# Performance work log

Hardware: AMD Instinct MI355X
Metric: run time of the kernel (lower is better)

## Reference

```python
import jax, jax.numpy as jnp
import numpy as np

STATE_DIM = 16
MEAS_DIM = 8
T = 500_000


def setup_inputs() -> dict:
    key = jax.random.key(0)
    k1, k2 = jax.random.split(key)
    measurements = jax.random.normal(k1, (T, MEAS_DIM, 1), dtype=jnp.float32)
    # F contracted slightly below identity so the 500k-step recursion stays stable
    F = 0.95 * jnp.eye(STATE_DIM, dtype=jnp.float32) \
        + 0.01 * jax.random.normal(k2, (STATE_DIM, STATE_DIM), dtype=jnp.float32)
    H = jnp.eye(MEAS_DIM, STATE_DIM, dtype=jnp.float32)  # matches nn.Parameter(torch.eye(m, n))
    Q = jnp.eye(STATE_DIM, dtype=jnp.float32)
    R = jnp.eye(MEAS_DIM, dtype=jnp.float32)
    return {"measurements": measurements, "F": F, "H": H, "Q": Q, "R": R}


def reference(measurements, F, H, Q, R):
    n = F.shape[0]
    I = jnp.eye(n, dtype=F.dtype)
    x0 = jnp.zeros((n, 1), dtype=F.dtype)   # self.x init
    P0 = jnp.eye(n, dtype=F.dtype)          # self.P init

    def step(carry, z):
        x, P = carry
        # predict
        x = F @ x
        P = F @ P @ F.T + Q
        # update
        y = z - H @ x                         # (m,1) innovation
        S = H @ P @ H.T + R                   # (m,m) innovation covariance
        K = P @ H.T @ jnp.linalg.inv(S)       # (n,m) Kalman gain (faithful to torch.linalg.inv)
        x = x + K @ y
        P = (I - K @ H) @ P
        return (x, P), x

    _, states = jax.lax.scan(step, (x0, P0), measurements)
    return states  # (T, n, 1)
```

## Files before the change

### kernel.cpp

```cpp
#include <hip/hip_runtime.h>


#define TT 500000
#define T0 40
#define L1 32
#define NCHUNK 15624
#define GH 8
#define OWN 64
#define NBLK2 245
#define NTHR (16 * (GH + OWN/2))

#define OFF_A    0
#define OFF_KR   256
#define OFF_AL   512
#define OFF_KH   784

#define FENCE_LDS() do { \
  asm volatile("s_waitcnt lgkmcnt(0)" ::: "memory"); \
  __builtin_amdgcn_sched_barrier(0); \
} while (0)

#define FMACDPP(d, x, a, S) \
  asm("v_fmac_f32_dpp %0, %1, %2 row_ror:" #S " row_mask:0xf bank_mask:0xf" \
      : "+v"(d) : "v"(x), "v"(a))
#define MULDPPD(d, x, a, dep, S) \
  asm("v_mul_f32_dpp %0, %1, %2 row_ror:" #S " row_mask:0xf bank_mask:0xf" \
      : "=v"(d) : "v"(x), "v"(a), "v"(dep))

__device__ __forceinline__ float rlf(float v, int lane) {
  return __int_as_float(__builtin_amdgcn_readlane(__float_as_int(v), lane));
}
__device__ __forceinline__ float bpermf(int byteaddr, float v) {
  return __int_as_float(__builtin_amdgcn_ds_bpermute(byteaddr, __float_as_int(v)));
}
template<int CTL> __device__ __forceinline__ float dppf(float x) {
  return __int_as_float(__builtin_amdgcn_update_dpp(
      0, __float_as_int(x), CTL, 0xF, 0xF, false));
}
#define QP1 0x39
#define QP2 0x4E
#define QP3 0x93

__device__ __forceinline__ unsigned long long rtclock() {
  unsigned long long t;
  asm volatile("s_memrealtime %0\n\ts_waitcnt lgkmcnt(0)" : "=s"(t));
  return t;
}

__device__ __forceinline__ int rot_dir() {
  int r = threadIdx.x & 15;
  int m = __builtin_amdgcn_update_dpp(0, r, 0x121, 0xF, 0xF, false);
  return (m - r) & 15;
}
__device__ __forceinline__ float mv16(const float a[16], float x) {
  float s0 = a[0] * x;
  float s1, s2, s3;
  MULDPPD(s1, x, a[1], s0, 1);
  MULDPPD(s2, x, a[2], s0, 2);
  MULDPPD(s3, x, a[3], s0, 3);
  FMACDPP(s0, x, a[4], 4);   FMACDPP(s1, x, a[5], 5);
  FMACDPP(s2, x, a[6], 6);   FMACDPP(s3, x, a[7], 7);
  FMACDPP(s0, x, a[8], 8);   FMACDPP(s1, x, a[9], 9);
  FMACDPP(s2, x, a[10], 10); FMACDPP(s3, x, a[11], 11);
  FMACDPP(s0, x, a[12], 12); FMACDPP(s1, x, a[13], 13);
  FMACDPP(s2, x, a[14], 14); FMACDPP(s3, x, a[15], 15);
  return (s0 + s1) + (s2 + s3);
}
__device__ __forceinline__ float stepAK(const float a[16], const float k8[8],
                                        float u, float zv) {
  float s0 = __builtin_fmaf(k8[0], zv, a[0] * u);
  float s1, s2, s3;
  MULDPPD(s1, u, a[1], s0, 1);
  MULDPPD(s2, u, a[2], s0, 2);
  MULDPPD(s3, u, a[3], s0, 3);
  FMACDPP(s0, u, a[4], 4);   FMACDPP(s1, u, a[5], 5);
  FMACDPP(s2, u, a[6], 6);   FMACDPP(s3, u, a[7], 7);
  FMACDPP(s0, u, a[8], 8);   FMACDPP(s1, u, a[9], 9);
  FMACDPP(s2, u, a[10], 10); FMACDPP(s3, u, a[11], 11);
  FMACDPP(s0, u, a[12], 12); FMACDPP(s1, u, a[13], 13);
  FMACDPP(s2, u, a[14], 14); FMACDPP(s3, u, a[15], 15);
  FMACDPP(s1, zv, k8[1], 1); FMACDPP(s2, zv, k8[2], 2);
  FMACDPP(s3, zv, k8[3], 3); FMACDPP(s0, zv, k8[4], 4);
  FMACDPP(s1, zv, k8[5], 5); FMACDPP(s2, zv, k8[6], 6);
  FMACDPP(s3, zv, k8[7], 7);
  return (s0 + s1) + (s2 + s3);
}
__device__ __forceinline__ void load16(const float* p, int r, float d[16]) {
  #pragma unroll
  for (int j = 0; j < 4; ++j) {
    float4 t = ((const float4*)p)[r*4 + j];
    d[4*j] = t.x; d[4*j+1] = t.y; d[4*j+2] = t.z; d[4*j+3] = t.w;
  }
}
__device__ __forceinline__ void loadkrf(const float* p, int r, float k8[8]) {
  float kr[16];
  load16(p, r, kr);
  #pragma unroll
  for (int i = 0; i < 8; ++i) k8[i] = kr[i] + kr[i + 8];
}
__device__ __forceinline__ void loadz(const float* __restrict__ z, int s0_,
                                      int rr, float zr[L1]) {
  const float* zp = z + (size_t)s0_ * 8 + (rr & 7);
  if (s0_ + L1 <= TT) {
    #pragma unroll
    for (int t = 0; t < L1; ++t) zr[t] = zp[t * 8];
  } else {
    #pragma unroll
    for (int t = 0; t < L1; ++t) {
      const float* q = (s0_ + t < TT) ? (zp + t * 8) : z;
      zr[t] = *q;
    }
  }
}

__global__ __launch_bounds__(64) void kf_ricc(
    const float* __restrict__ Fg, const float* __restrict__ Qg,
    const float* __restrict__ Rg, float* __restrict__ ws)
{
  const int bid = blockIdx.x;
  if (bid != 0) {
    unsigned long long t0c = rtclock();
    float x = 1.0f + (float)threadIdx.x * 1e-7f;
    #pragma unroll 1
    for (int it = 0; it < 250; ++it) {
      #pragma unroll
      for (int j = 0; j < 48; ++j)
        x = __builtin_fmaf(x, 1.0000001f, 1e-30f);
      if (rtclock() - t0c > 4000ull) break;
    }
    asm volatile("" :: "v"(x));
    return;
  }

  const int l  = threadIdx.x;
  const int r4 = l >> 2;
  const int q  = l & 3;
  const int c4 = q * 4;
  const int dir = rot_dir();

  __shared__ float Ps[16][20], Pbs[16][20], Ms[16][20];
  __shared__ float KsL[16][8];

  float frow[16];
  #pragma unroll
  for (int k = 0; k < 16; ++k) frow[k] = Fg[r4*16 + k];
  float4 ftr[16];
  #pragma unroll
  for (int d = 0; d < 4; ++d) {
    #pragma unroll
    for (int jp = 0; jp < 4; ++jp) {
      int col = 4*((q + d) & 3) + jp;
      ftr[d*4+jp] = make_float4(Fg[(c4+0)*16 + col], Fg[(c4+1)*16 + col],
                                Fg[(c4+2)*16 + col], Fg[(c4+3)*16 + col]);
    }
  }
  float4 qreg = *(const float4*)&Qg[r4*16 + c4];
  float rcol[8];
  {
    int cc = l & 7;
    #pragma unroll
    for (int i = 0; i < 8; ++i) rcol[i] = Rg[i*8 + cc];
  }
  *(float4*)&Ps[r4][c4] = make_float4(r4==c4 ?1.f:0.f, r4==c4+1?1.f:0.f,
                                      r4==c4+2?1.f:0.f, r4==c4+3?1.f:0.f);
  const int  cidx = (l < 8) ? l : ((l < 24) ? (l - 8) : (l & 7));
  const bool isS  = (l < 8);
  const bool isB  = (l >= 8 && l < 24);
  const int  bj   = l - 8;
  const int  ba   = (8 + r4) << 2;
  float v[8];
  FENCE_LDS();

  for (int t = 0; t < T0; ++t) {
    float m0=0.f,m1=0.f,m2=0.f,m3=0.f;
    #pragma unroll
    for (int k = 0; k < 16; ++k) {
      float4 pk = *(const float4*)&Ps[k][c4];
      float f = frow[k];
      m0 += f*pk.x; m1 += f*pk.y; m2 += f*pk.z; m3 += f*pk.w;
    }
    float g1x=dppf<QP1>(m0), g1y=dppf<QP1>(m1), g1z=dppf<QP1>(m2), g1w=dppf<QP1>(m3);
    float g2x=dppf<QP2>(m0), g2y=dppf<QP2>(m1), g2z=dppf<QP2>(m2), g2w=dppf<QP2>(m3);
    float g3x=dppf<QP3>(m0), g3y=dppf<QP3>(m1), g3z=dppf<QP3>(m2), g3w=dppf<QP3>(m3);
    const float mq[4][4] = {{m0,m1,m2,m3},{g1x,g1y,g1z,g1w},
                            {g2x,g2y,g2z,g2w},{g3x,g3y,g3z,g3w}};
    float b0=qreg.x, b1=qreg.y, b2=qreg.z, b3=qreg.w;
    #pragma unroll
    for (int d = 0; d < 4; ++d) {
      #pragma unroll
      for (int jp = 0; jp < 4; ++jp) {
        float mm = mq[d][jp];
        float4 ft = ftr[d*4+jp];
        b0 += mm*ft.x; b1 += mm*ft.y; b2 += mm*ft.z; b3 += mm*ft.w;
      }
    }
    float4 pb = make_float4(b0,b1,b2,b3);
    *(float4*)&Pbs[r4][c4] = pb;
    FENCE_LDS();
    #pragma unroll
    for (int i = 0; i < 8; ++i)
      v[i] = Pbs[i][cidx] + (isS ? rcol[i] : 0.f);
    #pragma unroll
    for (int p = 0; p < 8; ++p) {
      float piv = rlf(v[p], p);
      float rc  = __builtin_amdgcn_rcpf(piv);
      float fi[8];
      #pragma unroll
      for (int i = 0; i < 8; ++i) fi[i] = rlf(v[i], p) * rc;
      #pragma unroll
      for (int i = 0; i < 8; ++i) if (i != p) v[i] -= fi[i] * v[p];
    }
    {
      float dv[8];
      #pragma unroll
      for (int i = 0; i < 8; ++i) dv[i] = __builtin_amdgcn_rcpf(rlf(v[i], i));
      #pragma unroll
      for (int i = 0; i < 8; ++i) v[i] *= dv[i];
    }
    if (isB) {
      #pragma unroll
      for (int i = 0; i < 8; ++i) ws[OFF_KH + t*128 + bj*8 + i] = v[i];
    }
    float kk[8];
    #pragma unroll
    for (int i = 0; i < 8; ++i) kk[i] = bpermf(ba, v[i]);
    float4 pn = pb;
    #pragma unroll
    for (int k = 0; k < 8; ++k) {
      float4 pr = *(const float4*)&Pbs[k][c4];
      float kv = kk[k];
      pn.x -= kv*pr.x; pn.y -= kv*pr.y; pn.z -= kv*pr.z; pn.w -= kv*pr.w;
    }
    *(float4*)&Ps[r4][c4] = pn;
    FENCE_LDS();
  }

  if (isB) {
    #pragma unroll
    for (int i = 0; i < 8; ++i) KsL[bj][i] = v[i];
  }
  float kk[8];
  #pragma unroll
  for (int i = 0; i < 8; ++i) kk[i] = bpermf(ba, v[i]);
  float a[4];
  #pragma unroll
  for (int j = 0; j < 4; ++j) {
    float s = Fg[r4*16 + c4 + j];
    #pragma unroll
    for (int k = 0; k < 8; ++k) s -= kk[k] * Fg[k*16 + c4 + j];
    a[j] = s;
  }
  *(float4*)&Ms[r4][c4] = make_float4(a[0],a[1],a[2],a[3]);
  #pragma unroll
  for (int j = 0; j < 4; ++j) {
    int c = c4 + j;
    int s = ((c - r4) * dir) & 15;
    ws[OFF_A + r4*16 + s] = a[j];
  }
  FENCE_LDS();
  if (l < 16) {
    #pragma unroll
    for (int s = 0; s < 16; ++s) {
      int c = (l + s*dir) & 15;
      ws[OFF_KR + l*16 + s] = (c < 8) ? KsL[l][c] : 0.f;
    }
  }
  FENCE_LDS();
  for (int n = 0; n < 5; ++n) {
    float (*src)[20] = (n & 1) ? Pbs : Ms;
    float (*dst)[20] = (n & 1) ? Ms : Pbs;
    float b[4] = {0.f, 0.f, 0.f, 0.f};
    #pragma unroll
    for (int k = 0; k < 16; ++k) {
      float m = src[r4][k];
      const float* p = &src[k][c4];
      b[0] += m*p[0]; b[1] += m*p[1]; b[2] += m*p[2]; b[3] += m*p[3];
    }
    FENCE_LDS();
    dst[r4][c4]=b[0]; dst[r4][c4+1]=b[1]; dst[r4][c4+2]=b[2]; dst[r4][c4+3]=b[3];
    FENCE_LDS();
    if (n == 4) {
      #pragma unroll
      for (int j = 0; j < 4; ++j) {
        int c = c4 + j;
        int s = ((c - r4) * dir) & 15;
        ws[OFF_AL + r4*16 + s] = b[j];
      }
    }
  }
}

__global__ __launch_bounds__(NTHR) void kf_scan(
    const float* __restrict__ z, const float* __restrict__ Fg,
    float* __restrict__ ws, float* __restrict__ out)
{
  const int tid = threadIdx.x;
  const int bid = blockIdx.x;
  const int r = tid & 15;
  const int g = tid >> 4;

  __shared__ float ueL[(GH + OWN) * 16];
  __shared__ float X0s[16];

  float a[16], krf[8];
  load16(&ws[OFF_A], r, a);
  loadkrf(&ws[OFF_KR], r, krf);

  float zrA[L1], zrB[L1];
  int cA = -1, cB = -1, lenB = 0, s0A = 0, s0B = 0;

  if (g < GH) {
    if (bid == 0) {
      if (g == 0) {
        float f[16];
        #pragma unroll
        for (int i = 0; i < 16; ++i) f[i] = Fg[r*16 + i];
        const float4* zb = (const float4*)z + r;
        const float4* kh = (const float4*)&ws[OFF_KH] + r*2;
        float x = 0.f;
        float4 d0 = zb[0], d1 = zb[16];
        float4 ka0 = kh[0],  kb0 = kh[1];
        float4 ka1 = kh[32], kb1 = kh[33];
        for (int b = 0; b < T0/8; ++b) {
          float4 nx = (b + 2 < T0/8) ? zb[(b+2)*16] : make_float4(0.f,0.f,0.f,0.f);
          #pragma unroll
          for (int j = 0; j < 8; ++j) {
            const int t = b*8 + j;
            float p0=0.f,p1=0.f,p2=0.f,p3=0.f;
            #pragma unroll
            for (int k = 0; k < 16; k += 4) {
              p0 += f[k]   * __shfl(x, k, 16);
              p1 += f[k+1] * __shfl(x, k+1, 16);
              p2 += f[k+2] * __shfl(x, k+2, 16);
              p3 += f[k+3] * __shfl(x, k+3, 16);
            }
            float xp = (p0+p1)+(p2+p3);
            float z0=__shfl(d0.x,2*j,16),   z1=__shfl(d0.y,2*j,16);
            float z2=__shfl(d0.z,2*j,16),   z3=__shfl(d0.w,2*j,16);
            float z4=__shfl(d0.x,2*j+1,16), z5=__shfl(d0.y,2*j+1,16);
            float z6=__shfl(d0.z,2*j+1,16), z7=__shfl(d0.w,2*j+1,16);
            float acc = xp;
            acc += ka0.x * (z0 - __shfl(xp,0,16));
            acc += ka0.y * (z1 - __shfl(xp,1,16));
            acc += ka0.z * (z2 - __shfl(xp,2,16));
            acc += ka0.w * (z3 - __shfl(xp,3,16));
            acc += kb0.x * (z4 - __shfl(xp,4,16));
            acc += kb0.y * (z5 - __shfl(xp,5,16));
            acc += kb0.z * (z6 - __shfl(xp,6,16));
            acc += kb0.w * (z7 - __shfl(xp,7,16));
            x = acc;
            out[t*16 + r] = x;
            ka0 = ka1; kb0 = kb1;
            if (t + 2 < T0) { ka1 = kh[(t+2)*32]; kb1 = kh[(t+2)*32 + 1]; }
          }
          d0 = d1; d1 = nx;
        }
        X0s[r] = x;
      }
    } else {
      int cg = bid*OWN - GH + g;
      int s0_ = T0 + cg*L1;
      loadz(z, s0_, r, zrA);
      float u = 0.f;
      #pragma unroll
      for (int t = 0; t < L1; ++t) u = stepAK(a, krf, u, zrA[t]);
      ueL[g*16 + r] = u;
    }
  } else {
    int k = g - GH;
    cA = bid*OWN + 2*k;
    if (cA < NCHUNK) {
      s0A = T0 + cA*L1;
      loadz(z, s0A, r, zrA);
      float u = 0.f;
      #pragma unroll
      for (int t = 0; t < L1; ++t) {
        u = stepAK(a, krf, u, zrA[t]);
        zrA[t] = u;
      }
      ueL[(GH + 2*k)*16 + r] = u;
      cB = cA + 1;
      if (cB < NCHUNK) {
        s0B = s0A + L1;
        lenB = min(s0B + L1, TT) - s0B;
        loadz(z, s0B, r, zrB);
        u = 0.f;
        #pragma unroll
        for (int t = 0; t < L1; ++t) {
          if (t >= lenB) break;
          u = stepAK(a, krf, u, zrB[t]);
          zrB[t] = u;
        }
        ueL[(GH + 2*k + 1)*16 + r] = u;
      }
    } else {
      cA = -1;
    }
  }
  float al[16];
  load16(&ws[OFF_AL], r, al);
  __syncthreads();

  if (cA >= 0) {
    const int kp2 = 2*(g - GH);
    float v = 0.f;
    if (cA >= GH) {
      float w8[GH];
      #pragma unroll
      for (int mm = 0; mm < GH; ++mm) w8[mm] = ueL[(kp2 + mm)*16 + r];
      #pragma unroll
      for (int mm = 0; mm < GH; ++mm) v = mv16(al, v) + w8[mm];
    } else {
      v = X0s[r];
      for (int j = 0; j < cA; ++j)
        v = mv16(al, v) + ueL[(GH + j)*16 + r];
    }
    float w = v;
    #pragma unroll
    for (int t = 0; t < L1; ++t) {
      w = mv16(a, w);
      out[(size_t)(s0A + t)*16 + r] = zrA[t] + w;
    }
    if (cB < NCHUNK && cB >= 0) {
      w = zrA[L1-1] + w;
      #pragma unroll
      for (int t = 0; t < L1; ++t) {
        if (t >= lenB) break;
        w = mv16(a, w);
        out[(size_t)(s0B + t)*16 + r] = zrB[t] + w;
      }
    }
  }
}

extern "C" void kernel_launch(void* const* d_in, const int* in_sizes, int n_in,
                              void* d_out, int out_size, void* d_ws, size_t ws_size,
                              hipStream_t stream) {
  const float* z  = (const float*)d_in[0];
  const float* Fg = (const float*)d_in[1];
  const float* Qg = (const float*)d_in[3];
  const float* Rg = (const float*)d_in[4];
  float* out = (float*)d_out;
  float* ws  = (float*)d_ws;

  kf_ricc<<<NBLK2, 64, 0, stream>>>(Fg, Qg, Rg, ws);
  kf_scan<<<NBLK2, NTHR, 0, stream>>>(z, Fg, ws, out);
}
```

Measured before the change: 74.74 us.

## Process three chunks per thread group in scan and simplify Gauss-Jordan inversion

Each 16-lane group in the scan kernel now handles three consecutive chunks instead of two, so blocks own 96 chunks and 163 blocks are launched instead of 245. This amortises the 8-chunk ghost prefix work and the alpha-propagation over more owned chunks, at the cost of longer serial per-thread chains and more registers (a third 32-element buffer). The Riccati kernel's Gauss-Jordan inversion is also rewritten to normalise the pivot row first, dropping the temporary factor array and the final diagonal division pass.

```diff
diff --git a/kernel.cpp b/kernel.cpp
--- a/kernel.cpp
+++ b/kernel.cpp
@@ -6,9 +6,10 @@
 #define L1 32
 #define NCHUNK 15624
 #define GH 8
-#define OWN 64
-#define NBLK2 245
-#define NTHR (16 * (GH + OWN/2))
+#define OWN 96
+#define NBLKR 245
+#define NBLKS 163
+#define NTHR (16 * (GH + OWN/3))
 
 #define OFF_A    0
 #define OFF_KR   256
@@ -202,20 +203,11 @@
       v[i] = Pbs[i][cidx] + (isS ? rcol[i] : 0.f);
     #pragma unroll
     for (int p = 0; p < 8; ++p) {
-      float piv = rlf(v[p], p);
-      float rc  = __builtin_amdgcn_rcpf(piv);
-      float fi[8];
-      #pragma unroll
-      for (int i = 0; i < 8; ++i) fi[i] = rlf(v[i], p) * rc;
-      #pragma unroll
-      for (int i = 0; i < 8; ++i) if (i != p) v[i] -= fi[i] * v[p];
-    }
-    {
-      float dv[8];
-      #pragma unroll
-      for (int i = 0; i < 8; ++i) dv[i] = __builtin_amdgcn_rcpf(rlf(v[i], i));
-      #pragma unroll
-      for (int i = 0; i < 8; ++i) v[i] *= dv[i];
+      float rc = __builtin_amdgcn_rcpf(rlf(v[p], p));
+      v[p] *= rc;
+      #pragma unroll
+      for (int i = 0; i < 8; ++i)
+        if (i != p) v[i] -= rlf(v[i], p) * v[p];
     }
     if (isB) {
       #pragma unroll
@@ -306,8 +298,8 @@
   load16(&ws[OFF_A], r, a);
   loadkrf(&ws[OFF_KR], r, krf);
 
-  float zrA[L1], zrB[L1];
-  int cA = -1, cB = -1, lenB = 0, s0A = 0, s0B = 0;
+  float zrA[L1], zrB[L1], zrC[L1];
+  int cA = -1, cB = -1, cC = -1, lenC = 0, s0A = 0;
 
   if (g < GH) {
     if (bid == 0) {
@@ -368,7 +360,7 @@
     }
   } else {
     int k = g - GH;
-    cA = bid*OWN + 2*k;
+    cA = bid*OWN + 3*k;
     if (cA < NCHUNK) {
       s0A = T0 + cA*L1;
       loadz(z, s0A, r, zrA);
@@ -378,21 +370,32 @@
         u = stepAK(a, krf, u, zrA[t]);
         zrA[t] = u;
       }
-      ueL[(GH + 2*k)*16 + r] = u;
+      ueL[(GH + 3*k)*16 + r] = u;
       cB = cA + 1;
       if (cB < NCHUNK) {
-        s0B = s0A + L1;
-        lenB = min(s0B + L1, TT) - s0B;
-        loadz(z, s0B, r, zrB);
+        loadz(z, s0A + L1, r, zrB);
         u = 0.f;
         #pragma unroll
         for (int t = 0; t < L1; ++t) {
-          if (t >= lenB) break;
           u = stepAK(a, krf, u, zrB[t]);
           zrB[t] = u;
         }
-        ueL[(GH + 2*k + 1)*16 + r] = u;
-      }
+        ueL[(GH + 3*k + 1)*16 + r] = u;
+        cC = cA + 2;
+        if (cC < NCHUNK) {
+          int s0C = s0A + 2*L1;
+          lenC = min(s0C + L1, TT) - s0C;
+          loadz(z, s0C, r, zrC);
+          u = 0.f;
+          #pragma unroll
+          for (int t = 0; t < L1; ++t) {
+            if (t >= lenC) break;
+            u = stepAK(a, krf, u, zrC[t]);
+            zrC[t] = u;
+          }
+          ueL[(GH + 3*k + 2)*16 + r] = u;
+        } else cC = -1;
+      } else { cB = -1; }
     } else {
       cA = -1;
     }
@@ -402,14 +405,14 @@
   __syncthreads();
 
   if (cA >= 0) {
-    const int kp2 = 2*(g - GH);
+    const int kp = 3*(g - GH);
     float v = 0.f;
     if (cA >= GH) {
       float w8[GH];
       #pragma unroll
-      for (int mm = 0; mm < GH; ++mm) w8[mm] = ueL[(kp2 + mm)*16 + r];
-      #pragma unroll
-      for (int mm = 0; mm < GH; ++mm) v = mv16(al, v) + w8[mm];
+      for (int m = 0; m < GH; ++m) w8[m] = ueL[(kp + m)*16 + r];
+      #pragma unroll
+      for (int m = 0; m < GH; ++m) v = mv16(al, v) + w8[m];
     } else {
       v = X0s[r];
       for (int j = 0; j < cA; ++j)
@@ -421,13 +424,23 @@
       w = mv16(a, w);
       out[(size_t)(s0A + t)*16 + r] = zrA[t] + w;
     }
-    if (cB < NCHUNK && cB >= 0) {
+    if (cB >= 0) {
       w = zrA[L1-1] + w;
+      const int s0B = s0A + L1;
       #pragma unroll
       for (int t = 0; t < L1; ++t) {
-        if (t >= lenB) break;
         w = mv16(a, w);
         out[(size_t)(s0B + t)*16 + r] = zrB[t] + w;
+      }
+      if (cC >= 0) {
+        w = zrB[L1-1] + w;
+        const int s0C = s0A + 2*L1;
+        #pragma unroll
+        for (int t = 0; t < L1; ++t) {
+          if (t >= lenC) break;
+          w = mv16(a, w);
+          out[(size_t)(s0C + t)*16 + r] = zrC[t] + w;
+        }
       }
     }
   }
@@ -443,6 +456,6 @@
   float* out = (float*)d_out;
   float* ws  = (float*)d_ws;
 
-  kf_ricc<<<NBLK2, 64, 0, stream>>>(Fg, Qg, Rg, ws);
-  kf_scan<<<NBLK2, NTHR, 0, stream>>>(z, Fg, ws, out);
-}
+  kf_ricc<<<NBLKR, 64, 0, stream>>>(Fg, Qg, Rg, ws);
+  kf_scan<<<NBLKS, NTHR, 0, stream>>>(z, Fg, ws, out);
+}
```

After: 80.85 us. 1.08x slower.
